# Optimization experiments

Measured on AMD Instinct MI355X. Metric: run time of the kernel, lower is better.

Reference implementation:

```python
import jax, jax.numpy as jnp
import numpy as np

N = 8            # n_qubits
N_LAYERS_CRZ = 1

_H = jnp.array([[1.0, 1.0], [1.0, -1.0]], dtype=jnp.complex64) / np.sqrt(2).astype(np.float32)
_X2 = jnp.array([[0.0, 1.0], [1.0, 0.0]], dtype=jnp.complex64)
_I2 = jnp.eye(2, dtype=jnp.complex64)


def _apply_1q(state, U, q):
    # shared (2,2) gate on wire q; state: (B, 2,...,2)
    moved = jnp.moveaxis(state, 1 + q, -1)
    out = jnp.einsum('ij,...j->...i', U, moved)
    return jnp.moveaxis(out, -1, 1 + q)


def _apply_1q_batched(state, U, q):
    # per-sample (B,2,2) gate on wire q
    moved = jnp.moveaxis(state, 1 + q, -1)
    out = jnp.einsum('bij,b...j->b...i', U, moved)
    return jnp.moveaxis(out, -1, 1 + q)


def _apply_diag_batched(state, d, q):
    # per-sample diagonal (B,2) phases on wire q
    shape = (d.shape[0],) + (1,) * q + (2,) + (1,) * (N - 1 - q)
    return state * d.reshape(shape)


def _apply_ctrl_diag(state, ph, c, t):
    # controlled diagonal: apply phases ph (2,) on target t when control c == 1
    moved = jnp.moveaxis(state, (1 + c, 1 + t), (-2, -1))
    d = jnp.stack([jnp.ones(2, state.dtype), ph])  # (bc, bt)
    moved = moved * d
    return jnp.moveaxis(moved, (-2, -1), (1 + c, 1 + t))


def _apply_ctrl(state, U, c, t):
    # controlled (2,2) gate, control c, target t
    moved = jnp.moveaxis(state, (1 + c, 1 + t), (-2, -1))
    s0 = moved[..., 0, :]
    s1 = jnp.einsum('ij,...j->...i', U, moved[..., 1, :])
    out = jnp.stack([s0, s1], axis=-2)
    return jnp.moveaxis(out, (-2, -1), (1 + c, 1 + t))


def _circuit(X, weights):
    B = X.shape[0]
    state = jnp.zeros((B,) + (2,) * N, jnp.complex64)
    state = state.at[(slice(None),) + (0,) * N].set(1.0)

    # encoding: H, RZ(x[2q]), RY(x[2q+1]) on each wire q (2q+1 < 16 always)
    for q in range(N):
        state = _apply_1q(state, _H, q)
        th_z = X[:, 2 * q]
        d = jnp.stack([jnp.exp(-0.5j * th_z), jnp.exp(0.5j * th_z)], axis=-1)  # (B,2)
        state = _apply_diag_batched(state, d, q)
        half = 0.5 * X[:, 2 * q + 1]
        c, s = jnp.cos(half), jnp.sin(half)
        Ury = jnp.stack([jnp.stack([c, -s], -1), jnp.stack([s, c], -1)], -2)  # (B,2,2) real
        state = _apply_1q_batched(state, Ury, q)

    # CRZ ring
    for l in range(N_LAYERS_CRZ):
        for i in range(N):
            th = weights[l, i]
            ph = jnp.stack([jnp.exp(-0.5j * th), jnp.exp(0.5j * th)])
            state = _apply_ctrl_diag(state, ph, i, (i + 1) % N)

    # all-to-all CRX
    for i in range(N):
        for j in range(N):
            if j == i:
                continue
            half = 0.5 * weights[N_LAYERS_CRZ + i, j]
            Urx = jnp.cos(half) * _I2 + (-1j * jnp.sin(half)) * _X2
            state = _apply_ctrl(state, Urx, i, j)

    probs = jnp.real(state * jnp.conj(state)).reshape(B, 2 ** N)
    q_idx = jnp.arange(N)
    bits = (jnp.arange(2 ** N)[None, :] >> (N - 1 - q_idx)[:, None]) & 1  # (N, 2^N)
    signs = (1.0 - 2.0 * bits).astype(probs.dtype)
    return probs @ signs.T  # (B, N) <Z_q> expectations


def setup_inputs() -> dict:
    key = jax.random.key(0)
    k1, k2 = jax.random.split(key)
    X = jax.random.normal(k1, (16384, 2 * N), dtype=jnp.float32)
    weights = jax.random.normal(k2, (N_LAYERS_CRZ + N, (N_LAYERS_CRZ + N) * N), dtype=jnp.float32)
    return {"X": X, "weights": weights}


def reference(X, weights):
    return _circuit(X, weights)
```

## Files before the change

### kernel.cpp

```cpp
#include <hip/hip_runtime.h>


static __device__ __forceinline__ float rlane(float v, int src) {
    return __int_as_float(__builtin_amdgcn_readlane(__float_as_int(v), src));
}
template <int CTRL>
static __device__ __forceinline__ float dppf(float x) {
    return __int_as_float(__builtin_amdgcn_update_dpp(0, __float_as_int(x), CTRL, 0xF, 0xF, true));
}
static __device__ __forceinline__ float xor1f(float x) { return dppf<0xB1>(x); }
static __device__ __forceinline__ float xor2f(float x) { return dppf<0x4E>(x); }
static __device__ __forceinline__ float xor4f(float x) { return dppf<0x1B>(dppf<0x141>(x)); }
static __device__ __forceinline__ float xor8f(float x) { return dppf<0x128>(x); }
static __device__ __forceinline__ float xorMf(float x, int m) {
    if (m == 1) return xor1f(x);
    if (m == 2) return xor2f(x);
    if (m == 4) return xor4f(x);
    return xor8f(x);
}
static __device__ __forceinline__ float2 xorM2(float2 a, int m) {
    float2 t; t.x = xorMf(a.x, m); t.y = xorMf(a.y, m); return t;
}
static __device__ __forceinline__ float2 cmul(float2 a, float2 b) {
    float2 t;
    t.x = a.x * b.x - a.y * b.y;
    t.y = a.x * b.y + a.y * b.x;
    return t;
}
static __device__ __forceinline__ float2 rotA(float2 t, float2 u, float c, float s) {
    float2 d;
    d.x = c * t.x + s * u.y;
    d.y = c * t.y - s * u.x;
    return d;
}

__global__ __launch_bounds__(1024, 4) void qsim_kernel(const float* __restrict__ X,
                                                       const float* __restrict__ W,
                                                       float* __restrict__ out,
                                                       int B) {
    const int lane = threadIdx.x & 63;
    const int warp = threadIdx.x >> 6;
    const int g = lane >> 4;
    const int s = lane & 15;
    const int b = (blockIdx.x * 16 + warp) * 4 + g;
    const bool active = (b < B);
    const int bc = active ? b : (B - 1);

    float gcv = 1.0f, gsv = 0.0f;
    if (lane < 56) {
        const int i = lane / 7;
        const int jj = lane - 7 * i;
        const int j = jj + (jj >= i ? 1 : 0);
        const float h = 0.5f * W[(1 + i) * 72 + j];
        __sincosf(h, &gsv, &gcv);
    }

    float u0r, u0i, u1r, u1i;
    {
        const int q = s & 7;
        float2 xq = ((const float2*)X)[bc * 8 + q];
        float cz, sz, cy, sy;
        __sincosf(0.5f * xq.x, &sz, &cz);
        __sincosf(0.5f * xq.y, &sy, &cy);
        u0r = (cy - sy) * cz;  u0i = -(cy + sy) * sz;
        u1r = (cy + sy) * cz;  u1i = (cy - sy) * sz;
    }

    float2 P; P.x = 1.0f; P.y = 0.0f;
#pragma unroll
    for (int q = 4; q < 8; ++q) {
        const int src = (g << 4) + q;
        const float a0r = __shfl(u0r, src, 64), a0i = __shfl(u0i, src, 64);
        const float a1r = __shfl(u1r, src, 64), a1i = __shfl(u1i, src, 64);
        const int bit = (s >> (7 - q)) & 1;
        float2 v; v.x = bit ? a1r : a0r; v.y = bit ? a1i : a0i;
        P = cmul(P, v);
    }
    float2 w0[4], w1[4];
#pragma unroll
    for (int k = 0; k < 4; ++k) {
        const int src = (g << 4) + k;
        w0[k].x = __shfl(u0r, src, 64);  w0[k].y = __shfl(u0i, src, 64);
        w1[k].x = __shfl(u1r, src, 64);  w1[k].y = __shfl(u1i, src, 64);
    }
    float2 a[16];
    {
        float2 t1[2];
        t1[0] = w0[0];
        t1[1] = w1[0];
        float2 t2[4];
#pragma unroll
        for (int h = 0; h < 2; ++h) {
            t2[h * 2 + 0] = cmul(t1[h], w0[1]);
            t2[h * 2 + 1] = cmul(t1[h], w1[1]);
        }
        float2 t3[8];
#pragma unroll
        for (int h = 0; h < 4; ++h) {
            t3[h * 2 + 0] = cmul(t2[h], w0[2]);
            t3[h * 2 + 1] = cmul(t2[h], w1[2]);
        }
#pragma unroll
        for (int h = 0; h < 8; ++h) {
            a[h * 2 + 0] = cmul(P, cmul(t3[h], w0[3]));
            a[h * 2 + 1] = cmul(P, cmul(t3[h], w1[3]));
        }
    }

    {
        const float wv0 = W[0], wv1 = W[1], wv2 = W[2], wv3 = W[3];
        const float wv4 = W[4], wv5 = W[5], wv6 = W[6], wv7 = W[7];
        const int s3 = (s >> 3) & 1, s2 = (s >> 2) & 1, s1 = (s >> 1) & 1, s0 = s & 1;
        float phiS = 0.0f;
        phiS += s3 ? (s2 ? wv4 : -wv4) : 0.0f;
        phiS += s2 ? (s1 ? wv5 : -wv5) : 0.0f;
        phiS += s1 ? (s0 ? wv6 : -wv6) : 0.0f;
        const float termA = s3 ? wv3 : -wv3;
        const float termB = s0 ? wv7 : 0.0f;
#pragma unroll
        for (int r = 0; r < 16; ++r) {
            const int b3 = (r >> 3) & 1, b2 = (r >> 2) & 1, b1 = (r >> 1) & 1, b0 = r & 1;
            float phi = phiS + (b3 ? termB : -termB);
            if (b3) phi += b2 ? wv0 : -wv0;
            if (b2) phi += b1 ? wv1 : -wv1;
            if (b1) phi += b0 ? wv2 : -wv2;
            if (b0) phi += termA;
            float2 ph;
            __sincosf(0.5f * phi, &ph.y, &ph.x);
            a[r] = cmul(a[r], ph);
        }
    }

#pragma unroll
    for (int i = 0; i < 4; ++i) {
        float cg[8], sg[8];
#pragma unroll
        for (int j = 0; j < 8; ++j) {
            if (j == i) continue;
            const int gi = i * 7 + (j < i ? j : j - 1);
            cg[j] = rlane(gcv, gi);
            sg[j] = rlane(gsv, gi);
        }
        const int rc = 3 - i;
#pragma unroll
        for (int j = 0; j < 8; ++j) {
            if (j == i) continue;
            if (j < 4) {
                const int mt = 1 << (3 - j);
#pragma unroll
                for (int r = 0; r < 16; ++r) {
                    if (!((r >> rc) & 1)) continue;
                    if (r & mt) continue;
                    const int rp = r | mt;
                    const float2 t = a[r], u = a[rp];
                    a[r]  = rotA(t, u, cg[j], sg[j]);
                    a[rp] = rotA(u, t, cg[j], sg[j]);
                }
            } else {
                const int ms = 1 << (7 - j);
#pragma unroll
                for (int r = 0; r < 16; ++r) {
                    if (!((r >> rc) & 1)) continue;
                    const float2 p = xorM2(a[r], ms);
                    a[r] = rotA(a[r], p, cg[j], sg[j]);
                }
            }
        }
    }

#pragma unroll
    for (int k = 1; k <= 8; k <<= 1) {
        const bool sk = (s & k) != 0;
#pragma unroll
        for (int r = 0; r < 16; ++r) {
            if (r & k) continue;
            const int rp = r | k;
            const float2 tp = xorM2(a[rp], k);
            const float2 tr = xorM2(a[r],  k);
            a[r].x  = sk ? tp.x : a[r].x;
            a[r].y  = sk ? tp.y : a[r].y;
            a[rp].x = sk ? a[rp].x : tr.x;
            a[rp].y = sk ? a[rp].y : tr.y;
        }
    }

#pragma unroll
    for (int i = 4; i < 8; ++i) {
        float cg[8], sg[8];
#pragma unroll
        for (int j = 0; j < 8; ++j) {
            if (j == i) continue;
            const int gi = i * 7 + (j < i ? j : j - 1);
            cg[j] = rlane(gcv, gi);
            sg[j] = rlane(gsv, gi);
        }
        const int rc = 7 - i;
#pragma unroll
        for (int j = 0; j < 8; ++j) {
            if (j == i) continue;
            if (j < 4) {
                const int ms = 1 << (3 - j);
#pragma unroll
                for (int r = 0; r < 16; ++r) {
                    if (!((r >> rc) & 1)) continue;
                    const float2 p = xorM2(a[r], ms);
                    a[r] = rotA(a[r], p, cg[j], sg[j]);
                }
            } else {
                const int mt = 1 << (7 - j);
#pragma unroll
                for (int r = 0; r < 16; ++r) {
                    if (!((r >> rc) & 1)) continue;
                    if (r & mt) continue;
                    const int rp = r | mt;
                    const float2 t = a[r], u = a[rp];
                    a[r]  = rotA(t, u, cg[j], sg[j]);
                    a[rp] = rotA(u, t, cg[j], sg[j]);
                }
            }
        }
    }

    float p[16];
#pragma unroll
    for (int r = 0; r < 16; ++r) p[r] = a[r].x * a[r].x + a[r].y * a[r].y;
    float s8[8], E7 = 0.0f;
#pragma unroll
    for (int k = 0; k < 8; ++k) { s8[k] = p[2 * k] + p[2 * k + 1]; E7 += p[2 * k] - p[2 * k + 1]; }
    float s4[4], E6 = 0.0f;
#pragma unroll
    for (int k = 0; k < 4; ++k) { s4[k] = s8[2 * k] + s8[2 * k + 1]; E6 += s8[2 * k] - s8[2 * k + 1]; }
    float s2a[2], E5 = 0.0f;
#pragma unroll
    for (int k = 0; k < 2; ++k) { s2a[k] = s4[2 * k] + s4[2 * k + 1]; E5 += s4[2 * k] - s4[2 * k + 1]; }
    float A  = s2a[0] + s2a[1];
    float E4 = s2a[0] - s2a[1];
    float D0, D1, D2, D3;
    { const float t = xor1f(A); D0 = A - t; A += t;
      E4 += xor1f(E4); E5 += xor1f(E5); E6 += xor1f(E6); E7 += xor1f(E7); }
    { const float t = xor2f(A); D1 = A - t; A += t;
      D0 += xor2f(D0);
      E4 += xor2f(E4); E5 += xor2f(E5); E6 += xor2f(E6); E7 += xor2f(E7); }
    { const float t = xor4f(A); D2 = A - t; A += t;
      D0 += xor4f(D0); D1 += xor4f(D1);
      E4 += xor4f(E4); E5 += xor4f(E5); E6 += xor4f(E6); E7 += xor4f(E7); }
    { const float t = xor8f(A); D3 = A - t;
      D0 += xor8f(D0); D1 += xor8f(D1); D2 += xor8f(D2);
      E4 += xor8f(E4); E5 += xor8f(E5); E6 += xor8f(E6); E7 += xor8f(E7); }

    if (s == 0 && active) {
        const float sc = 1.0f / 256.0f;
        float* o = out + b * 8;
        o[0] = D3 * sc;
        o[1] = D2 * sc;
        o[2] = D1 * sc;
        o[3] = D0 * sc;
        o[4] = E4 * sc;
        o[5] = E5 * sc;
        o[6] = E6 * sc;
        o[7] = E7 * sc;
    }
}

extern "C" void kernel_launch(void* const* d_in, const int* in_sizes, int n_in,
                              void* d_out, int out_size, void* d_ws, size_t ws_size,
                              hipStream_t stream) {
    const float* X = (const float*)d_in[0];
    const float* W = (const float*)d_in[1];
    float* out = (float*)d_out;
    const int B = in_sizes[0] / 16;
    const int blocks = (B + 63) / 64;
    qsim_kernel<<<blocks, 1024, 0, stream>>>(X, W, out, B);
}
```

Baseline: 76.59 us.

## Spread each sample's state over 32 lanes with 8 amplitudes per lane

```diff
diff --git a/kernel.cpp b/kernel.cpp
--- a/kernel.cpp
+++ b/kernel.cpp
@@ -12,14 +12,20 @@
 static __device__ __forceinline__ float xor2f(float x) { return dppf<0x4E>(x); }
 static __device__ __forceinline__ float xor4f(float x) { return dppf<0x1B>(dppf<0x141>(x)); }
 static __device__ __forceinline__ float xor8f(float x) { return dppf<0x128>(x); }
-static __device__ __forceinline__ float xorMf(float x, int m) {
-    if (m == 1) return xor1f(x);
-    if (m == 2) return xor2f(x);
-    if (m == 4) return xor4f(x);
-    return xor8f(x);
-}
-static __device__ __forceinline__ float2 xorM2(float2 a, int m) {
-    float2 t; t.x = xorMf(a.x, m); t.y = xorMf(a.y, m); return t;
+static __device__ __forceinline__ float swz16f(float x) {
+    return __int_as_float(__builtin_amdgcn_ds_swizzle(__float_as_int(x), 0x401F));
+}
+template <int MS>
+static __device__ __forceinline__ float xorT(float x) {
+    if constexpr (MS == 1) return xor1f(x);
+    else if constexpr (MS == 2) return xor2f(x);
+    else if constexpr (MS == 4) return xor4f(x);
+    else if constexpr (MS == 8) return xor8f(x);
+    else return swz16f(x);
+}
+template <int MS>
+static __device__ __forceinline__ float2 xorT2(float2 v) {
+    float2 t; t.x = xorT<MS>(v.x); t.y = xorT<MS>(v.y); return t;
 }
 static __device__ __forceinline__ float2 cmul(float2 a, float2 b) {
     float2 t;
@@ -33,16 +39,62 @@
     d.y = c * t.y - s * u.x;
     return d;
 }
-
-__global__ __launch_bounds__(1024, 4) void qsim_kernel(const float* __restrict__ X,
-                                                       const float* __restrict__ W,
-                                                       float* __restrict__ out,
-                                                       int B) {
+template <int MS>
+static __device__ __forceinline__ void crxLane1(float2& ar, float c, float sv) {
+    const float px = xorT<MS>(ar.x);
+    const float py = xorT<MS>(ar.y);
+    const float mx = py * sv;
+    const float my = px * sv;
+    ar.x = __builtin_fmaf(c, ar.x, mx);
+    ar.y = __builtin_fmaf(c, ar.y, -my);
+}
+template <int RC, int MT>
+static __device__ __forceinline__ void crxReg(float2 (&a)[8], float c, float s) {
+#pragma unroll
+    for (int r = 0; r < 8; ++r) {
+        if (!((r >> RC) & 1)) continue;
+        if (r & MT) continue;
+        const int rp = r | MT;
+        const float2 t = a[r], u = a[rp];
+        a[r]  = rotA(t, u, c, s);
+        a[rp] = rotA(u, t, c, s);
+    }
+}
+template <int RC, int MS>
+static __device__ __forceinline__ void crxLaneG(float2 (&a)[8], float c, float sv) {
+#pragma unroll
+    for (int r = 0; r < 8; ++r) {
+        if (!((r >> RC) & 1)) continue;
+        crxLane1<MS>(a[r], c, sv);
+    }
+}
+template <int MT, int MS>
+static __device__ __forceinline__ void transposeStage(float2 (&a)[8], int s) {
+    const bool sk = (s & MS) != 0;
+#pragma unroll
+    for (int r = 0; r < 8; ++r) {
+        if (r & MT) continue;
+        const int rp = r | MT;
+        const float2 tp = xorT2<MS>(a[rp]);
+        const float2 tr = xorT2<MS>(a[r]);
+        a[r].x  = sk ? tp.x : a[r].x;
+        a[r].y  = sk ? tp.y : a[r].y;
+        a[rp].x = sk ? a[rp].x : tr.x;
+        a[rp].y = sk ? a[rp].y : tr.y;
+    }
+}
+
+#define G(gi) rlane(gcv, gi), rlane(gsv, gi)
+
+__global__ __launch_bounds__(256, 8) void qsim_kernel(const float* __restrict__ X,
+                                                      const float* __restrict__ W,
+                                                      float* __restrict__ out,
+                                                      int B) {
     const int lane = threadIdx.x & 63;
-    const int warp = threadIdx.x >> 6;
-    const int g = lane >> 4;
-    const int s = lane & 15;
-    const int b = (blockIdx.x * 16 + warp) * 4 + g;
+    const int wv = threadIdx.x >> 6;
+    const int e = lane >> 5;
+    const int s = lane & 31;
+    const int b = (blockIdx.x * 4 + wv) * 2 + e;
     const bool active = (b < B);
     const int bc = active ? b : (B - 1);
 
@@ -68,22 +120,22 @@
 
     float2 P; P.x = 1.0f; P.y = 0.0f;
 #pragma unroll
-    for (int q = 4; q < 8; ++q) {
-        const int src = (g << 4) + q;
+    for (int q = 3; q < 8; ++q) {
+        const int src = (e << 5) + q;
         const float a0r = __shfl(u0r, src, 64), a0i = __shfl(u0i, src, 64);
         const float a1r = __shfl(u1r, src, 64), a1i = __shfl(u1i, src, 64);
         const int bit = (s >> (7 - q)) & 1;
         float2 v; v.x = bit ? a1r : a0r; v.y = bit ? a1i : a0i;
         P = cmul(P, v);
     }
-    float2 w0[4], w1[4];
-#pragma unroll
-    for (int k = 0; k < 4; ++k) {
-        const int src = (g << 4) + k;
+    float2 w0[3], w1[3];
+#pragma unroll
+    for (int k = 0; k < 3; ++k) {
+        const int src = (e << 5) + k;
         w0[k].x = __shfl(u0r, src, 64);  w0[k].y = __shfl(u0i, src, 64);
         w1[k].x = __shfl(u1r, src, 64);  w1[k].y = __shfl(u1i, src, 64);
     }
-    float2 a[16];
+    float2 a[8];
     {
         float2 t1[2];
         t1[0] = w0[0];
@@ -94,171 +146,139 @@
             t2[h * 2 + 0] = cmul(t1[h], w0[1]);
             t2[h * 2 + 1] = cmul(t1[h], w1[1]);
         }
-        float2 t3[8];
 #pragma unroll
         for (int h = 0; h < 4; ++h) {
-            t3[h * 2 + 0] = cmul(t2[h], w0[2]);
-            t3[h * 2 + 1] = cmul(t2[h], w1[2]);
-        }
-#pragma unroll
-        for (int h = 0; h < 8; ++h) {
-            a[h * 2 + 0] = cmul(P, cmul(t3[h], w0[3]));
-            a[h * 2 + 1] = cmul(P, cmul(t3[h], w1[3]));
+            a[h * 2 + 0] = cmul(P, cmul(t2[h], w0[2]));
+            a[h * 2 + 1] = cmul(P, cmul(t2[h], w1[2]));
         }
     }
 
     {
         const float wv0 = W[0], wv1 = W[1], wv2 = W[2], wv3 = W[3];
         const float wv4 = W[4], wv5 = W[5], wv6 = W[6], wv7 = W[7];
-        const int s3 = (s >> 3) & 1, s2 = (s >> 2) & 1, s1 = (s >> 1) & 1, s0 = s & 1;
+        const int s4b = (s >> 4) & 1, s3b = (s >> 3) & 1, s2b = (s >> 2) & 1,
+                  s1b = (s >> 1) & 1, s0b = s & 1;
         float phiS = 0.0f;
-        phiS += s3 ? (s2 ? wv4 : -wv4) : 0.0f;
-        phiS += s2 ? (s1 ? wv5 : -wv5) : 0.0f;
-        phiS += s1 ? (s0 ? wv6 : -wv6) : 0.0f;
-        const float termA = s3 ? wv3 : -wv3;
-        const float termB = s0 ? wv7 : 0.0f;
-#pragma unroll
-        for (int r = 0; r < 16; ++r) {
-            const int b3 = (r >> 3) & 1, b2 = (r >> 2) & 1, b1 = (r >> 1) & 1, b0 = r & 1;
-            float phi = phiS + (b3 ? termB : -termB);
-            if (b3) phi += b2 ? wv0 : -wv0;
-            if (b2) phi += b1 ? wv1 : -wv1;
-            if (b1) phi += b0 ? wv2 : -wv2;
-            if (b0) phi += termA;
+        phiS += s4b ? (s3b ? wv3 : -wv3) : 0.0f;
+        phiS += s3b ? (s2b ? wv4 : -wv4) : 0.0f;
+        phiS += s2b ? (s1b ? wv5 : -wv5) : 0.0f;
+        phiS += s1b ? (s0b ? wv6 : -wv6) : 0.0f;
+        const float termB = s0b ? wv7 : 0.0f;
+        const float termC = s4b ? wv2 : -wv2;
+#pragma unroll
+        for (int r = 0; r < 8; ++r) {
+            const int r2 = (r >> 2) & 1, r1 = (r >> 1) & 1, r0 = r & 1;
+            float phi = phiS + (r2 ? termB : -termB);
+            if (r2) phi += r1 ? wv0 : -wv0;
+            if (r1) phi += r0 ? wv1 : -wv1;
+            if (r0) phi += termC;
             float2 ph;
             __sincosf(0.5f * phi, &ph.y, &ph.x);
             a[r] = cmul(a[r], ph);
         }
     }
 
-#pragma unroll
-    for (int i = 0; i < 4; ++i) {
-        float cg[8], sg[8];
-#pragma unroll
-        for (int j = 0; j < 8; ++j) {
-            if (j == i) continue;
-            const int gi = i * 7 + (j < i ? j : j - 1);
-            cg[j] = rlane(gcv, gi);
-            sg[j] = rlane(gsv, gi);
-        }
-        const int rc = 3 - i;
-#pragma unroll
-        for (int j = 0; j < 8; ++j) {
-            if (j == i) continue;
-            if (j < 4) {
-                const int mt = 1 << (3 - j);
-#pragma unroll
-                for (int r = 0; r < 16; ++r) {
-                    if (!((r >> rc) & 1)) continue;
-                    if (r & mt) continue;
-                    const int rp = r | mt;
-                    const float2 t = a[r], u = a[rp];
-                    a[r]  = rotA(t, u, cg[j], sg[j]);
-                    a[rp] = rotA(u, t, cg[j], sg[j]);
-                }
-            } else {
-                const int ms = 1 << (7 - j);
-#pragma unroll
-                for (int r = 0; r < 16; ++r) {
-                    if (!((r >> rc) & 1)) continue;
-                    const float2 p = xorM2(a[r], ms);
-                    a[r] = rotA(a[r], p, cg[j], sg[j]);
-                }
-            }
-        }
-    }
-
-#pragma unroll
-    for (int k = 1; k <= 8; k <<= 1) {
-        const bool sk = (s & k) != 0;
-#pragma unroll
-        for (int r = 0; r < 16; ++r) {
-            if (r & k) continue;
-            const int rp = r | k;
-            const float2 tp = xorM2(a[rp], k);
-            const float2 tr = xorM2(a[r],  k);
-            a[r].x  = sk ? tp.x : a[r].x;
-            a[r].y  = sk ? tp.y : a[r].y;
-            a[rp].x = sk ? a[rp].x : tr.x;
-            a[rp].y = sk ? a[rp].y : tr.y;
-        }
-    }
-
-#pragma unroll
-    for (int i = 4; i < 8; ++i) {
-        float cg[8], sg[8];
-#pragma unroll
-        for (int j = 0; j < 8; ++j) {
-            if (j == i) continue;
-            const int gi = i * 7 + (j < i ? j : j - 1);
-            cg[j] = rlane(gcv, gi);
-            sg[j] = rlane(gsv, gi);
-        }
-        const int rc = 7 - i;
-#pragma unroll
-        for (int j = 0; j < 8; ++j) {
-            if (j == i) continue;
-            if (j < 4) {
-                const int ms = 1 << (3 - j);
-#pragma unroll
-                for (int r = 0; r < 16; ++r) {
-                    if (!((r >> rc) & 1)) continue;
-                    const float2 p = xorM2(a[r], ms);
-                    a[r] = rotA(a[r], p, cg[j], sg[j]);
-                }
-            } else {
-                const int mt = 1 << (7 - j);
-#pragma unroll
-                for (int r = 0; r < 16; ++r) {
-                    if (!((r >> rc) & 1)) continue;
-                    if (r & mt) continue;
-                    const int rp = r | mt;
-                    const float2 t = a[r], u = a[rp];
-                    a[r]  = rotA(t, u, cg[j], sg[j]);
-                    a[rp] = rotA(u, t, cg[j], sg[j]);
-                }
-            }
-        }
-    }
-
-    float p[16];
-#pragma unroll
-    for (int r = 0; r < 16; ++r) p[r] = a[r].x * a[r].x + a[r].y * a[r].y;
-    float s8[8], E7 = 0.0f;
-#pragma unroll
-    for (int k = 0; k < 8; ++k) { s8[k] = p[2 * k] + p[2 * k + 1]; E7 += p[2 * k] - p[2 * k + 1]; }
-    float s4[4], E6 = 0.0f;
-#pragma unroll
-    for (int k = 0; k < 4; ++k) { s4[k] = s8[2 * k] + s8[2 * k + 1]; E6 += s8[2 * k] - s8[2 * k + 1]; }
-    float s2a[2], E5 = 0.0f;
-#pragma unroll
-    for (int k = 0; k < 2; ++k) { s2a[k] = s4[2 * k] + s4[2 * k + 1]; E5 += s4[2 * k] - s4[2 * k + 1]; }
-    float A  = s2a[0] + s2a[1];
-    float E4 = s2a[0] - s2a[1];
-    float D0, D1, D2, D3;
-    { const float t = xor1f(A); D0 = A - t; A += t;
-      E4 += xor1f(E4); E5 += xor1f(E5); E6 += xor1f(E6); E7 += xor1f(E7); }
-    { const float t = xor2f(A); D1 = A - t; A += t;
-      D0 += xor2f(D0);
-      E4 += xor2f(E4); E5 += xor2f(E5); E6 += xor2f(E6); E7 += xor2f(E7); }
-    { const float t = xor4f(A); D2 = A - t; A += t;
-      D0 += xor4f(D0); D1 += xor4f(D1);
-      E4 += xor4f(E4); E5 += xor4f(E5); E6 += xor4f(E6); E7 += xor4f(E7); }
-    { const float t = xor8f(A); D3 = A - t;
-      D0 += xor8f(D0); D1 += xor8f(D1); D2 += xor8f(D2);
-      E4 += xor8f(E4); E5 += xor8f(E5); E6 += xor8f(E6); E7 += xor8f(E7); }
+    crxReg<2, 2>(a, G(0));
+    crxReg<2, 1>(a, G(1));
+    crxLaneG<2, 16>(a, G(2));
+    crxLaneG<2, 8>(a, G(3));
+    crxLaneG<2, 4>(a, G(4));
+    crxLaneG<2, 2>(a, G(5));
+    crxLaneG<2, 1>(a, G(6));
+    crxReg<1, 4>(a, G(7));
+    crxReg<1, 1>(a, G(8));
+    crxLaneG<1, 16>(a, G(9));
+    crxLaneG<1, 8>(a, G(10));
+    crxLaneG<1, 4>(a, G(11));
+    crxLaneG<1, 2>(a, G(12));
+    crxLaneG<1, 1>(a, G(13));
+    crxReg<0, 4>(a, G(14));
+    crxReg<0, 2>(a, G(15));
+    crxLaneG<0, 16>(a, G(16));
+    crxLaneG<0, 8>(a, G(17));
+    crxLaneG<0, 4>(a, G(18));
+    crxLaneG<0, 2>(a, G(19));
+    crxLaneG<0, 1>(a, G(20));
+
+    transposeStage<4, 16>(a, s);
+    transposeStage<2, 8>(a, s);
+    transposeStage<1, 4>(a, s);
+
+    crxLaneG<2, 16>(a, G(21));
+    crxLaneG<2, 8>(a, G(22));
+    crxLaneG<2, 4>(a, G(23));
+    crxReg<2, 2>(a, G(24));
+    crxReg<2, 1>(a, G(25));
+    crxLaneG<2, 2>(a, G(26));
+    crxLaneG<2, 1>(a, G(27));
+    crxLaneG<1, 16>(a, G(28));
+    crxLaneG<1, 8>(a, G(29));
+    crxLaneG<1, 4>(a, G(30));
+    crxReg<1, 4>(a, G(31));
+    crxReg<1, 1>(a, G(32));
+    crxLaneG<1, 2>(a, G(33));
+    crxLaneG<1, 1>(a, G(34));
+    crxLaneG<0, 16>(a, G(35));
+    crxLaneG<0, 8>(a, G(36));
+    crxLaneG<0, 4>(a, G(37));
+    crxReg<0, 4>(a, G(38));
+    crxReg<0, 2>(a, G(39));
+    crxLaneG<0, 2>(a, G(40));
+    crxLaneG<0, 1>(a, G(41));
+
+    transposeStage<2, 2>(a, s);
+    transposeStage<1, 1>(a, s);
+
+    crxLaneG<1, 16>(a, G(42));
+    crxLaneG<1, 8>(a, G(43));
+    crxLaneG<1, 4>(a, G(44));
+    crxReg<1, 4>(a, G(45));
+    crxLaneG<1, 2>(a, G(46));
+    crxLaneG<1, 1>(a, G(47));
+    crxReg<1, 1>(a, G(48));
+    crxLaneG<0, 16>(a, G(49));
+    crxLaneG<0, 8>(a, G(50));
+    crxLaneG<0, 4>(a, G(51));
+    crxReg<0, 4>(a, G(52));
+    crxLaneG<0, 2>(a, G(53));
+    crxLaneG<0, 1>(a, G(54));
+    crxReg<0, 2>(a, G(55));
+
+    float p[8];
+#pragma unroll
+    for (int r = 0; r < 8; ++r) p[r] = a[r].x * a[r].x + a[r].y * a[r].y;
+    float s4v[4], E7 = 0.0f;
+#pragma unroll
+    for (int k = 0; k < 4; ++k) { s4v[k] = p[2 * k] + p[2 * k + 1]; E7 += p[2 * k] - p[2 * k + 1]; }
+    float s2v[2], E6 = 0.0f;
+#pragma unroll
+    for (int k = 0; k < 2; ++k) { s2v[k] = s4v[2 * k] + s4v[2 * k + 1]; E6 += s4v[2 * k] - s4v[2 * k + 1]; }
+    float A  = s2v[0] + s2v[1];
+    float E3 = s2v[0] - s2v[1];
+    float Dq5, Dq4, Dq2, Dq1, Dq0;
+    { const float t = xor1f(A); Dq5 = A - t; A += t;
+      E3 += xor1f(E3); E6 += xor1f(E6); E7 += xor1f(E7); }
+    { const float t = xor2f(A); Dq4 = A - t; A += t;
+      Dq5 += xor2f(Dq5);
+      E3 += xor2f(E3); E6 += xor2f(E6); E7 += xor2f(E7); }
+    { const float t = xor4f(A); Dq2 = A - t; A += t;
+      Dq5 += xor4f(Dq5); Dq4 += xor4f(Dq4);
+      E3 += xor4f(E3); E6 += xor4f(E6); E7 += xor4f(E7); }
+    { const float t = xor8f(A); Dq1 = A - t; A += t;
+      Dq5 += xor8f(Dq5); Dq4 += xor8f(Dq4); Dq2 += xor8f(Dq2);
+      E3 += xor8f(E3); E6 += xor8f(E6); E7 += xor8f(E7); }
+    { const float t = swz16f(A); Dq0 = A - t;
+      Dq5 += swz16f(Dq5); Dq4 += swz16f(Dq4); Dq2 += swz16f(Dq2); Dq1 += swz16f(Dq1);
+      E3 += swz16f(E3); E6 += swz16f(E6); E7 += swz16f(E7); }
 
     if (s == 0 && active) {
         const float sc = 1.0f / 256.0f;
-        float* o = out + b * 8;
-        o[0] = D3 * sc;
-        o[1] = D2 * sc;
-        o[2] = D1 * sc;
-        o[3] = D0 * sc;
-        o[4] = E4 * sc;
-        o[5] = E5 * sc;
-        o[6] = E6 * sc;
-        o[7] = E7 * sc;
+        float4 o0, o1;
+        o0.x = Dq0 * sc; o0.y = Dq1 * sc; o0.z = Dq2 * sc; o0.w = E3 * sc;
+        o1.x = Dq4 * sc; o1.y = Dq5 * sc; o1.z = E6 * sc;  o1.w = E7 * sc;
+        float4* o = (float4*)(out + b * 8);
+        o[0] = o0;
+        o[1] = o1;
     }
 }
 
@@ -269,6 +289,6 @@
     const float* W = (const float*)d_in[1];
     float* out = (float*)d_out;
     const int B = in_sizes[0] / 16;
-    const int blocks = (B + 63) / 64;
-    qsim_kernel<<<blocks, 1024, 0, stream>>>(X, W, out, B);
-}
+    const int blocks = (B + 7) / 8;
+    qsim_kernel<<<blocks, 256, 0, stream>>>(X, W, out, B);
+}
```

Result: slower. 78.87 us (+3.0%).
